# Kernel tuning notes

Measured on AMD Instinct MI355X. Metric: run time of the kernel, lower is better.

The kernel has to match this reference:

```python
import jax, jax.numpy as jnp
import numpy as np

EMBED = 100
BATCH = 4096
NUM_NEG = 256
U, P, W, RP, B, C = 30000, 50000, 100000, 50000, 5000, 1000


def _tab(k, v, e=EMBED):
    r = 0.5 / e
    w = jax.random.uniform(k, (v + 1, e), minval=-r, maxval=r, dtype=jnp.float32)
    return w.at[-1].set(0.0)  # padding row is zeros, as in torch code


def setup_inputs() -> dict:
    key = jax.random.key(0)
    ks = jax.random.split(key, 10)
    inp = {
        'user_emb': _tab(ks[0], U),
        'product_emb': _tab(ks[1], P),
        'word_emb': _tab(ks[2], W),
        'brand_emb': _tab(ks[3], B),
        'category_emb': _tab(ks[4], C),
        'rproduct_emb': _tab(ks[5], RP),
        'rel_vecs': jax.random.uniform(ks[6], (8, EMBED), minval=-0.5 / EMBED, maxval=0.5 / EMBED, dtype=jnp.float32),
        'purchase_bias': jnp.zeros((P + 1,), jnp.float32),
        'mentions_bias': jnp.zeros((W + 1,), jnp.float32),
        'describe_bias': jnp.zeros((W + 1,), jnp.float32),
        'produced_bias': jnp.zeros((B + 1,), jnp.float32),
        'belongs_bias': jnp.zeros((C + 1,), jnp.float32),
        'also_bought_bias': jnp.zeros((RP + 1,), jnp.float32),
        'also_viewed_bias': jnp.zeros((RP + 1,), jnp.float32),
        'together_bias': jnp.zeros((RP + 1,), jnp.float32),
    }
    # batch_idxs columns: (u, p, w, b, c, rp1, rp2, rp3), each in its own vocab range
    col_max = [U, P, W, B, C, RP, RP, RP]
    cols = [jax.random.randint(jax.random.fold_in(ks[7], i), (BATCH,), 0, m) for i, m in enumerate(col_max)]
    inp['batch_idxs'] = jnp.stack(cols, axis=1)
    # deterministic stand-in for torch.multinomial negative sampling, one row per relation
    neg_max = [P, W, W, B, C, RP, RP, RP]
    negs = [jax.random.randint(jax.random.fold_in(ks[8], i), (NUM_NEG,), 0, m) for i, m in enumerate(neg_max)]
    inp['neg_idxs'] = jnp.stack(negs, axis=0)
    return inp


def _neg_loss(head_tab, tail_tab, rvec, bias_tab, h, t, n):
    hv = head_tab[h]                      # [B,E] gather
    ex = hv + rvec                        # [B,E]
    tv = tail_tab[t]                      # [B,E]
    bias = bias_tab[t]                    # [B]
    pos = jnp.sum(ex * tv, axis=-1) + bias  # bmm([B,1,E],[B,E,1]) == rowwise dot
    nv = tail_tab[n]                      # [N,E]
    neg = jnp.einsum('be,ne->bn', ex, nv) + bias[:, None]  # [B,N]
    pos_loss = -jax.nn.log_sigmoid(pos)   # == -log(sigmoid(pos)), stable
    neg_loss = -jax.nn.log_sigmoid(-neg).sum(axis=1)
    return (pos_loss + neg_loss).mean()


def reference(batch_idxs, neg_idxs, user_emb, product_emb, word_emb, brand_emb,
              category_emb, rproduct_emb, rel_vecs, purchase_bias, mentions_bias,
              describe_bias, produced_bias, belongs_bias, also_bought_bias,
              also_viewed_bias, together_bias):
    # (head_tab, tail_tab, bias_tab, head_col, tail_col) per relation, in original order
    rels = [
        (user_emb, product_emb, purchase_bias, 0, 1),
        (user_emb, word_emb, mentions_bias, 0, 2),
        (product_emb, word_emb, describe_bias, 1, 2),
        (product_emb, brand_emb, produced_bias, 1, 3),
        (product_emb, category_emb, belongs_bias, 1, 4),
        (product_emb, rproduct_emb, also_bought_bias, 1, 5),
        (product_emb, rproduct_emb, also_viewed_bias, 1, 6),
        (product_emb, rproduct_emb, together_bias, 1, 7),
    ]
    loss = jnp.float32(0.0)
    for r, (ht, tt, bt, hc, tc) in enumerate(rels):
        loss = loss + _neg_loss(ht, tt, rel_vecs[r], bt,
                                batch_idxs[:, hc], batch_idxs[:, tc], neg_idxs[r])
    return loss
```

## Files before the change

### kernel.cpp

```cpp
#include <hip/hip_runtime.h>


#define EMBED   100
#define BATCH   4096
#define NUM_NEG 256
#define BM      128
#define BN      128
#define PITCH   128

typedef __attribute__((ext_vector_type(8))) short s8;
typedef __attribute__((ext_vector_type(4))) float f4;

struct RelP {
    const float* head;
    const float* tail;
    const float* bias;
    int hc, tc;
};

struct Params {
    RelP rel[8];
    const float* rel_vecs;
    const int*   batch_idxs;
    const int*   neg_idxs;
    float*       out;
};

__device__ __forceinline__ float softplus_f(float x) {
    float e = __expf(-fabsf(x));
    return fmaxf(x, 0.0f) + __logf(1.0f + e);
}

__device__ __forceinline__ unsigned short bf16_rne(float f) {
    unsigned u = __float_as_uint(f);
    u += 0x7FFFu + ((u >> 16) & 1u);
    return (unsigned short)(u >> 16);
}

__device__ __forceinline__ float bf16_to_f(short s) {
    return __uint_as_float(((unsigned)(unsigned short)s) << 16);
}

__device__ __forceinline__ s8 pack8(float4 f0, float4 f1) {
    s8 v = { (short)bf16_rne(f0.x), (short)bf16_rne(f0.y),
             (short)bf16_rne(f0.z), (short)bf16_rne(f0.w),
             (short)bf16_rne(f1.x), (short)bf16_rne(f1.y),
             (short)bf16_rne(f1.z), (short)bf16_rne(f1.w) };
    return v;
}

__launch_bounds__(256, 2)
__global__ void ke_kernel(Params p) {
    const int bid = blockIdx.x;
    const int r   = bid & 7;
    const int rb  = (bid >> 3) & 31;
    const int nb  = bid >> 8;
    const int tid = threadIdx.x;

    __shared__ __align__(16) short As[BM * PITCH];
    __shared__ __align__(16) short Bs[BN * PITCH];

    const RelP rp = p.rel[r];

    {
        const bool isA = tid < BM;
        const int  row = isA ? tid : (tid - BM);
        const int  sw  = row & 7;
        const float* src;
        unsigned short extra;
        short* dst;
        if (isA) {
            const int grow = rb * BM + row;
            const int h  = p.batch_idxs[grow * 8 + rp.hc];
            const int ti = p.batch_idxs[grow * 8 + rp.tc];
            src   = rp.head + (size_t)h * EMBED;
            extra = bf16_rne(rp.bias[ti]);
            dst   = As + row * PITCH;
        } else {
            const int n = p.neg_idxs[r * NUM_NEG + nb * BN + row];
            src   = rp.tail + (size_t)n * EMBED;
            extra = 0x3F80;
            dst   = Bs + row * PITCH;
        }
        const float4* s4p = (const float4*)src;
        const float4* rv4 = (const float4*)(p.rel_vecs + r * EMBED);

#pragma unroll
        for (int c = 0; c < 12; ++c) {
            float4 f0 = s4p[2 * c];
            float4 f1 = s4p[2 * c + 1];
            if (isA) {
                const float4 a = rv4[2 * c];
                const float4 b = rv4[2 * c + 1];
                f0.x += a.x; f0.y += a.y; f0.z += a.z; f0.w += a.w;
                f1.x += b.x; f1.y += b.y; f1.z += b.z; f1.w += b.w;
            }
            *(s8*)(dst + 8 * (c ^ sw)) = pack8(f0, f1);
        }
        {
            float4 f = s4p[24];
            if (isA) {
                const float4 a = rv4[24];
                f.x += a.x; f.y += a.y; f.z += a.z; f.w += a.w;
            }
            s8 v = { (short)bf16_rne(f.x), (short)bf16_rne(f.y),
                     (short)bf16_rne(f.z), (short)bf16_rne(f.w),
                     (short)extra, 0, 0, 0 };
            *(s8*)(dst + 8 * (12 ^ sw)) = v;
        }
        {
            s8 z = {0,0,0,0,0,0,0,0};
            *(s8*)(dst + 8 * (13 ^ sw)) = z;
            *(s8*)(dst + 8 * (14 ^ sw)) = z;
            *(s8*)(dst + 8 * (15 ^ sw)) = z;
        }
    }

    const bool doPos = (nb == 0) && (tid >= BM);
    const float* ptail = rp.tail;
    float pbias = 0.0f;
    if (doPos) {
        const int prow = rb * BM + (tid - BM);
        const int pt = p.batch_idxs[prow * 8 + rp.tc];
        ptail = rp.tail + (size_t)pt * EMBED;
        pbias = rp.bias[pt];
    }

    __syncthreads();

    const int wave = tid >> 6;
    const int lane = tid & 63;
    const int li   = lane & 15;
    const int q    = lane >> 4;
    const int wm   = wave >> 1;
    const int wn   = wave & 1;
    const int sw   = li & 7;

    f4 acc[4][4];
#pragma unroll
    for (int i = 0; i < 4; ++i)
#pragma unroll
        for (int j = 0; j < 4; ++j)
            acc[i][j] = (f4){0.f, 0.f, 0.f, 0.f};

    const short* Abase = As + (wm * 64 + li) * PITCH;
    const short* Bbase = Bs + (wn * 64 + li) * PITCH;

#pragma unroll
    for (int s = 0; s < 4; ++s) {
        const int co = 8 * ((q + 4 * s) ^ sw);
        const s8 a0 = *(const s8*)(Abase +  0 * PITCH + co);
        const s8 a1 = *(const s8*)(Abase + 16 * PITCH + co);
        const s8 a2 = *(const s8*)(Abase + 32 * PITCH + co);
        const s8 a3 = *(const s8*)(Abase + 48 * PITCH + co);
        const s8 b0 = *(const s8*)(Bbase +  0 * PITCH + co);
        const s8 b1 = *(const s8*)(Bbase + 16 * PITCH + co);
        const s8 b2 = *(const s8*)(Bbase + 32 * PITCH + co);
        const s8 b3 = *(const s8*)(Bbase + 48 * PITCH + co);
        acc[0][0] = __builtin_amdgcn_mfma_f32_16x16x32_bf16(a0, b0, acc[0][0], 0, 0, 0);
        acc[0][1] = __builtin_amdgcn_mfma_f32_16x16x32_bf16(a0, b1, acc[0][1], 0, 0, 0);
        acc[0][2] = __builtin_amdgcn_mfma_f32_16x16x32_bf16(a0, b2, acc[0][2], 0, 0, 0);
        acc[0][3] = __builtin_amdgcn_mfma_f32_16x16x32_bf16(a0, b3, acc[0][3], 0, 0, 0);
        acc[1][0] = __builtin_amdgcn_mfma_f32_16x16x32_bf16(a1, b0, acc[1][0], 0, 0, 0);
        acc[1][1] = __builtin_amdgcn_mfma_f32_16x16x32_bf16(a1, b1, acc[1][1], 0, 0, 0);
        acc[1][2] = __builtin_amdgcn_mfma_f32_16x16x32_bf16(a1, b2, acc[1][2], 0, 0, 0);
        acc[1][3] = __builtin_amdgcn_mfma_f32_16x16x32_bf16(a1, b3, acc[1][3], 0, 0, 0);
        acc[2][0] = __builtin_amdgcn_mfma_f32_16x16x32_bf16(a2, b0, acc[2][0], 0, 0, 0);
        acc[2][1] = __builtin_amdgcn_mfma_f32_16x16x32_bf16(a2, b1, acc[2][1], 0, 0, 0);
        acc[2][2] = __builtin_amdgcn_mfma_f32_16x16x32_bf16(a2, b2, acc[2][2], 0, 0, 0);
        acc[2][3] = __builtin_amdgcn_mfma_f32_16x16x32_bf16(a2, b3, acc[2][3], 0, 0, 0);
        acc[3][0] = __builtin_amdgcn_mfma_f32_16x16x32_bf16(a3, b0, acc[3][0], 0, 0, 0);
        acc[3][1] = __builtin_amdgcn_mfma_f32_16x16x32_bf16(a3, b1, acc[3][1], 0, 0, 0);
        acc[3][2] = __builtin_amdgcn_mfma_f32_16x16x32_bf16(a3, b2, acc[3][2], 0, 0, 0);
        acc[3][3] = __builtin_amdgcn_mfma_f32_16x16x32_bf16(a3, b3, acc[3][3], 0, 0, 0);
    }

    float local = 0.0f;
#pragma unroll
    for (int i = 0; i < 4; ++i)
#pragma unroll
        for (int j = 0; j < 4; ++j) {
            local += softplus_f(acc[i][j].x);
            local += softplus_f(acc[i][j].y);
            local += softplus_f(acc[i][j].z);
            local += softplus_f(acc[i][j].w);
        }

    if (doPos) {
        const int prow = tid - BM;
        const int psw  = prow & 7;
        const short* exr = As + prow * PITCH;
        const float4* tv = (const float4*)ptail;
        float d0 = 0.f, d1 = 0.f, d2 = 0.f, d3 = 0.f;
#pragma unroll
        for (int c = 0; c < 12; ++c) {
            const s8 e = *(const s8*)(exr + 8 * (c ^ psw));
            const float4 t0 = tv[2 * c];
            const float4 t1 = tv[2 * c + 1];
            d0 = fmaf(bf16_to_f(e[0]), t0.x, d0);
            d1 = fmaf(bf16_to_f(e[1]), t0.y, d1);
            d2 = fmaf(bf16_to_f(e[2]), t0.z, d2);
            d3 = fmaf(bf16_to_f(e[3]), t0.w, d3);
            d0 = fmaf(bf16_to_f(e[4]), t1.x, d0);
            d1 = fmaf(bf16_to_f(e[5]), t1.y, d1);
            d2 = fmaf(bf16_to_f(e[6]), t1.z, d2);
            d3 = fmaf(bf16_to_f(e[7]), t1.w, d3);
        }
        {
            const s8 e = *(const s8*)(exr + 8 * (12 ^ psw));
            const float4 t0 = tv[24];
            d0 = fmaf(bf16_to_f(e[0]), t0.x, d0);
            d1 = fmaf(bf16_to_f(e[1]), t0.y, d1);
            d2 = fmaf(bf16_to_f(e[2]), t0.z, d2);
            d3 = fmaf(bf16_to_f(e[3]), t0.w, d3);
        }
        const float pos = ((d0 + d1) + (d2 + d3)) + pbias;
        local += softplus_f(-pos);
    }

#pragma unroll
    for (int off = 32; off > 0; off >>= 1)
        local += __shfl_down(local, off, 64);

    __syncthreads();
    float* wsum = (float*)Bs;
    const int lane2 = tid & 63;
    if (lane2 == 0) wsum[tid >> 6] = local;
    __syncthreads();
    if (tid == 0) {
        const float s = (wsum[0] + wsum[1]) + (wsum[2] + wsum[3]);
        atomicAdd(p.out, s * (1.0f / BATCH));
    }
}

extern "C" void kernel_launch(void* const* d_in, const int* in_sizes, int n_in,
                              void* d_out, int out_size, void* d_ws, size_t ws_size,
                              hipStream_t stream) {
    const float* user  = (const float*)d_in[0];
    const float* prod  = (const float*)d_in[1];
    const float* word  = (const float*)d_in[2];
    const float* brand = (const float*)d_in[3];
    const float* cat   = (const float*)d_in[4];
    const float* rprod = (const float*)d_in[5];

    Params p;
    p.rel_vecs   = (const float*)d_in[6];
    p.batch_idxs = (const int*)d_in[15];
    p.neg_idxs   = (const int*)d_in[16];
    p.out        = (float*)d_out;

    p.rel[0] = {user, prod,  (const float*)d_in[7],  0, 1};
    p.rel[1] = {user, word,  (const float*)d_in[8],  0, 2};
    p.rel[2] = {prod, word,  (const float*)d_in[9],  1, 2};
    p.rel[3] = {prod, brand, (const float*)d_in[10], 1, 3};
    p.rel[4] = {prod, cat,   (const float*)d_in[11], 1, 4};
    p.rel[5] = {prod, rprod, (const float*)d_in[12], 1, 5};
    p.rel[6] = {prod, rprod, (const float*)d_in[13], 1, 6};
    p.rel[7] = {prod, rprod, (const float*)d_in[14], 1, 7};

    hipMemsetAsync(d_out, 0, sizeof(float), stream);
    ke_kernel<<<512, 256, 0, stream>>>(p);
}
```

Measured before the change: 152.2 us.

## Halve row tile, trim K padding, and spread positive dot across negative blocks

Cuts the batch tile from 128 to 64 rows and doubles the grid to 1024 blocks, raising launch-bounds occupancy to 4 blocks per CU. The LDS pitch drops from 128 to 104 shorts, which removes the zero-padded K chunks and the XOR swizzle. The last MFMA step masks the upper lanes to zero. The positive-pair dot product is now split across both negative-block halves and four lanes per row, combined with shuffles. This trades less redundant staging and MFMA work and better balance for a possibly bank-conflicted unswizzled LDS layout and twice as many blocks, each reloading the tail tile.

```diff
diff --git a/kernel.cpp b/kernel.cpp
--- a/kernel.cpp
+++ b/kernel.cpp
@@ -4,9 +4,9 @@
 #define EMBED   100
 #define BATCH   4096
 #define NUM_NEG 256
-#define BM      128
+#define BM      64
 #define BN      128
-#define PITCH   128
+#define PITCH   104
 
 typedef __attribute__((ext_vector_type(8))) short s8;
 typedef __attribute__((ext_vector_type(4))) float f4;
@@ -49,12 +49,13 @@
     return v;
 }
 
-__launch_bounds__(256, 2)
+__launch_bounds__(256, 4)
 __global__ void ke_kernel(Params p) {
     const int bid = blockIdx.x;
     const int r   = bid & 7;
-    const int rb  = (bid >> 3) & 31;
-    const int nb  = bid >> 8;
+    const int x   = bid >> 3;
+    const int rb  = x & 63;
+    const int nb  = x >> 6;
     const int tid = threadIdx.x;
 
     __shared__ __align__(16) short As[BM * PITCH];
@@ -62,66 +63,61 @@
 
     const RelP rp = p.rel[r];
 
-    {
-        const bool isA = tid < BM;
-        const int  row = isA ? tid : (tid - BM);
-        const int  sw  = row & 7;
-        const float* src;
-        unsigned short extra;
-        short* dst;
-        if (isA) {
-            const int grow = rb * BM + row;
-            const int h  = p.batch_idxs[grow * 8 + rp.hc];
-            const int ti = p.batch_idxs[grow * 8 + rp.tc];
-            src   = rp.head + (size_t)h * EMBED;
-            extra = bf16_rne(rp.bias[ti]);
-            dst   = As + row * PITCH;
-        } else {
-            const int n = p.neg_idxs[r * NUM_NEG + nb * BN + row];
-            src   = rp.tail + (size_t)n * EMBED;
-            extra = 0x3F80;
-            dst   = Bs + row * PITCH;
-        }
-        const float4* s4p = (const float4*)src;
+    if (tid < BM) {
+        const int row  = tid;
+        const int grow = rb * BM + row;
+        const int h  = p.batch_idxs[grow * 8 + rp.hc];
+        const int ti = p.batch_idxs[grow * 8 + rp.tc];
+        const float4* s4p = (const float4*)(rp.head + (size_t)h * EMBED);
         const float4* rv4 = (const float4*)(p.rel_vecs + r * EMBED);
-
+        const unsigned short extra = bf16_rne(rp.bias[ti]);
+        short* dst = As + row * PITCH;
 #pragma unroll
         for (int c = 0; c < 12; ++c) {
             float4 f0 = s4p[2 * c];
             float4 f1 = s4p[2 * c + 1];
-            if (isA) {
-                const float4 a = rv4[2 * c];
-                const float4 b = rv4[2 * c + 1];
-                f0.x += a.x; f0.y += a.y; f0.z += a.z; f0.w += a.w;
-                f1.x += b.x; f1.y += b.y; f1.z += b.z; f1.w += b.w;
-            }
-            *(s8*)(dst + 8 * (c ^ sw)) = pack8(f0, f1);
+            const float4 a = rv4[2 * c];
+            const float4 b = rv4[2 * c + 1];
+            f0.x += a.x; f0.y += a.y; f0.z += a.z; f0.w += a.w;
+            f1.x += b.x; f1.y += b.y; f1.z += b.z; f1.w += b.w;
+            *(s8*)(dst + 8 * c) = pack8(f0, f1);
         }
         {
             float4 f = s4p[24];
-            if (isA) {
-                const float4 a = rv4[24];
-                f.x += a.x; f.y += a.y; f.z += a.z; f.w += a.w;
-            }
+            const float4 a = rv4[24];
+            f.x += a.x; f.y += a.y; f.z += a.z; f.w += a.w;
             s8 v = { (short)bf16_rne(f.x), (short)bf16_rne(f.y),
                      (short)bf16_rne(f.z), (short)bf16_rne(f.w),
                      (short)extra, 0, 0, 0 };
-            *(s8*)(dst + 8 * (12 ^ sw)) = v;
+            *(s8*)(dst + 96) = v;
+        }
+    } else if (tid < 192) {
+        const int row = tid - 64;
+        const int n = p.neg_idxs[r * NUM_NEG + nb * BN + row];
+        const float4* s4p = (const float4*)(rp.tail + (size_t)n * EMBED);
+        short* dst = Bs + row * PITCH;
+#pragma unroll
+        for (int c = 0; c < 12; ++c) {
+            float4 f0 = s4p[2 * c];
+            float4 f1 = s4p[2 * c + 1];
+            *(s8*)(dst + 8 * c) = pack8(f0, f1);
         }
         {
-            s8 z = {0,0,0,0,0,0,0,0};
-            *(s8*)(dst + 8 * (13 ^ sw)) = z;
-            *(s8*)(dst + 8 * (14 ^ sw)) = z;
-            *(s8*)(dst + 8 * (15 ^ sw)) = z;
-        }
-    }
-
-    const bool doPos = (nb == 0) && (tid >= BM);
+            float4 f = s4p[24];
+            s8 v = { (short)bf16_rne(f.x), (short)bf16_rne(f.y),
+                     (short)bf16_rne(f.z), (short)bf16_rne(f.w),
+                     (short)0x3F80, 0, 0, 0 };
+            *(s8*)(dst + 96) = v;
+        }
+    }
+
+    const bool doPos = tid >= 128;
     const float* ptail = rp.tail;
     float pbias = 0.0f;
     if (doPos) {
-        const int prow = rb * BM + (tid - BM);
-        const int pt = p.batch_idxs[prow * 8 + rp.tc];
+        const int pl   = tid - 128;
+        const int prow = rb * BM + nb * 32 + (pl >> 2);
+        const int pt   = p.batch_idxs[prow * 8 + rp.tc];
         ptail = rp.tail + (size_t)pt * EMBED;
         pbias = rp.bias[pt];
     }
@@ -134,50 +130,56 @@
     const int q    = lane >> 4;
     const int wm   = wave >> 1;
     const int wn   = wave & 1;
-    const int sw   = li & 7;
-
-    f4 acc[4][4];
-#pragma unroll
-    for (int i = 0; i < 4; ++i)
+
+    f4 acc[2][4];
+#pragma unroll
+    for (int i = 0; i < 2; ++i)
 #pragma unroll
         for (int j = 0; j < 4; ++j)
             acc[i][j] = (f4){0.f, 0.f, 0.f, 0.f};
 
-    const short* Abase = As + (wm * 64 + li) * PITCH;
-    const short* Bbase = Bs + (wn * 64 + li) * PITCH;
-
-#pragma unroll
-    for (int s = 0; s < 4; ++s) {
-        const int co = 8 * ((q + 4 * s) ^ sw);
-        const s8 a0 = *(const s8*)(Abase +  0 * PITCH + co);
-        const s8 a1 = *(const s8*)(Abase + 16 * PITCH + co);
-        const s8 a2 = *(const s8*)(Abase + 32 * PITCH + co);
-        const s8 a3 = *(const s8*)(Abase + 48 * PITCH + co);
-        const s8 b0 = *(const s8*)(Bbase +  0 * PITCH + co);
-        const s8 b1 = *(const s8*)(Bbase + 16 * PITCH + co);
-        const s8 b2 = *(const s8*)(Bbase + 32 * PITCH + co);
-        const s8 b3 = *(const s8*)(Bbase + 48 * PITCH + co);
-        acc[0][0] = __builtin_amdgcn_mfma_f32_16x16x32_bf16(a0, b0, acc[0][0], 0, 0, 0);
-        acc[0][1] = __builtin_amdgcn_mfma_f32_16x16x32_bf16(a0, b1, acc[0][1], 0, 0, 0);
-        acc[0][2] = __builtin_amdgcn_mfma_f32_16x16x32_bf16(a0, b2, acc[0][2], 0, 0, 0);
-        acc[0][3] = __builtin_amdgcn_mfma_f32_16x16x32_bf16(a0, b3, acc[0][3], 0, 0, 0);
-        acc[1][0] = __builtin_amdgcn_mfma_f32_16x16x32_bf16(a1, b0, acc[1][0], 0, 0, 0);
-        acc[1][1] = __builtin_amdgcn_mfma_f32_16x16x32_bf16(a1, b1, acc[1][1], 0, 0, 0);
-        acc[1][2] = __builtin_amdgcn_mfma_f32_16x16x32_bf16(a1, b2, acc[1][2], 0, 0, 0);
-        acc[1][3] = __builtin_amdgcn_mfma_f32_16x16x32_bf16(a1, b3, acc[1][3], 0, 0, 0);
-        acc[2][0] = __builtin_amdgcn_mfma_f32_16x16x32_bf16(a2, b0, acc[2][0], 0, 0, 0);
-        acc[2][1] = __builtin_amdgcn_mfma_f32_16x16x32_bf16(a2, b1, acc[2][1], 0, 0, 0);
-        acc[2][2] = __builtin_amdgcn_mfma_f32_16x16x32_bf16(a2, b2, acc[2][2], 0, 0, 0);
-        acc[2][3] = __builtin_amdgcn_mfma_f32_16x16x32_bf16(a2, b3, acc[2][3], 0, 0, 0);
-        acc[3][0] = __builtin_amdgcn_mfma_f32_16x16x32_bf16(a3, b0, acc[3][0], 0, 0, 0);
-        acc[3][1] = __builtin_amdgcn_mfma_f32_16x16x32_bf16(a3, b1, acc[3][1], 0, 0, 0);
-        acc[3][2] = __builtin_amdgcn_mfma_f32_16x16x32_bf16(a3, b2, acc[3][2], 0, 0, 0);
-        acc[3][3] = __builtin_amdgcn_mfma_f32_16x16x32_bf16(a3, b3, acc[3][3], 0, 0, 0);
+    const short* Ab = As + (wm * 32 + li) * PITCH;
+    const short* Bb = Bs + (wn * 64 + li) * PITCH;
+
+#pragma unroll
+    for (int s = 0; s < 3; ++s) {
+        const int co = 8 * (q + 4 * s);
+        s8 a[2], b[4];
+        a[0] = *(const s8*)(Ab + co);
+        a[1] = *(const s8*)(Ab + 16 * PITCH + co);
+        b[0] = *(const s8*)(Bb + co);
+        b[1] = *(const s8*)(Bb + 16 * PITCH + co);
+        b[2] = *(const s8*)(Bb + 32 * PITCH + co);
+        b[3] = *(const s8*)(Bb + 48 * PITCH + co);
+#pragma unroll
+        for (int i = 0; i < 2; ++i)
+#pragma unroll
+            for (int j = 0; j < 4; ++j)
+                acc[i][j] = __builtin_amdgcn_mfma_f32_16x16x32_bf16(a[i], b[j], acc[i][j], 0, 0, 0);
+    }
+    {
+        const s8 z = {0, 0, 0, 0, 0, 0, 0, 0};
+        s8 a[2], b[4];
+        a[0] = *(const s8*)(Ab + 96);
+        a[1] = *(const s8*)(Ab + 16 * PITCH + 96);
+        b[0] = *(const s8*)(Bb + 96);
+        b[1] = *(const s8*)(Bb + 16 * PITCH + 96);
+        b[2] = *(const s8*)(Bb + 32 * PITCH + 96);
+        b[3] = *(const s8*)(Bb + 48 * PITCH + 96);
+        b[0] = q ? z : b[0];
+        b[1] = q ? z : b[1];
+        b[2] = q ? z : b[2];
+        b[3] = q ? z : b[3];
+#pragma unroll
+        for (int i = 0; i < 2; ++i)
+#pragma unroll
+            for (int j = 0; j < 4; ++j)
+                acc[i][j] = __builtin_amdgcn_mfma_f32_16x16x32_bf16(a[i], b[j], acc[i][j], 0, 0, 0);
     }
 
     float local = 0.0f;
 #pragma unroll
-    for (int i = 0; i < 4; ++i)
+    for (int i = 0; i < 2; ++i)
 #pragma unroll
         for (int j = 0; j < 4; ++j) {
             local += softplus_f(acc[i][j].x);
@@ -187,14 +189,17 @@
         }
 
     if (doPos) {
-        const int prow = tid - BM;
-        const int psw  = prow & 7;
-        const short* exr = As + prow * PITCH;
+        const int pl   = tid - 128;
+        const int prl  = pl >> 2;
+        const int part = pl & 3;
+        const short* exr = As + (nb * 32 + prl) * PITCH;
         const float4* tv = (const float4*)ptail;
         float d0 = 0.f, d1 = 0.f, d2 = 0.f, d3 = 0.f;
-#pragma unroll
-        for (int c = 0; c < 12; ++c) {
-            const s8 e = *(const s8*)(exr + 8 * (c ^ psw));
+        const int cbase = 3 * part;
+#pragma unroll
+        for (int k = 0; k < 3; ++k) {
+            const int c = cbase + k;
+            const s8 e = *(const s8*)(exr + 8 * c);
             const float4 t0 = tv[2 * c];
             const float4 t1 = tv[2 * c + 1];
             d0 = fmaf(bf16_to_f(e[0]), t0.x, d0);
@@ -206,16 +211,18 @@
             d2 = fmaf(bf16_to_f(e[6]), t1.z, d2);
             d3 = fmaf(bf16_to_f(e[7]), t1.w, d3);
         }
-        {
-            const s8 e = *(const s8*)(exr + 8 * (12 ^ psw));
+        if (part == 3) {
+            const s8 e = *(const s8*)(exr + 96);
             const float4 t0 = tv[24];
             d0 = fmaf(bf16_to_f(e[0]), t0.x, d0);
             d1 = fmaf(bf16_to_f(e[1]), t0.y, d1);
             d2 = fmaf(bf16_to_f(e[2]), t0.z, d2);
             d3 = fmaf(bf16_to_f(e[3]), t0.w, d3);
         }
-        const float pos = ((d0 + d1) + (d2 + d3)) + pbias;
-        local += softplus_f(-pos);
+        float d = (d0 + d1) + (d2 + d3);
+        d += __shfl_xor(d, 1, 64);
+        d += __shfl_xor(d, 2, 64);
+        if (part == 0) local += softplus_f(-(d + pbias));
     }
 
 #pragma unroll
@@ -224,8 +231,7 @@
 
     __syncthreads();
     float* wsum = (float*)Bs;
-    const int lane2 = tid & 63;
-    if (lane2 == 0) wsum[tid >> 6] = local;
+    if ((tid & 63) == 0) wsum[tid >> 6] = local;
     __syncthreads();
     if (tid == 0) {
         const float s = (wsum[0] + wsum[1]) + (wsum[2] + wsum[3]);
@@ -259,5 +265,5 @@
     p.rel[7] = {prod, rprod, (const float*)d_in[14], 1, 7};
 
     hipMemsetAsync(d_out, 0, sizeof(float), stream);
-    ke_kernel<<<512, 256, 0, stream>>>(p);
-}
+    ke_kernel<<<1024, 256, 0, stream>>>(p);
+}
```

New measurement: 153.8 us. Within noise of the previous version (+1.0%).
